# Kernel optimization log

Measured on AMD Instinct MI355X. Metric: run time of the kernel, lower is better.

Reference implementation:

```python
import jax, jax.numpy as jnp
import numpy as np

EPS_DEMOD = 1e-8
EPS_GN = 1e-5
GROUPS = 8


def setup_inputs() -> dict:
    key = jax.random.key(0)
    ks = jax.random.split(key, 4)
    b, c, h, w = 16, 64, 256, 256
    n_kernels, c_out = 4, 64
    x = jax.random.normal(ks[0], (b, c, h, w), dtype=jnp.float32)
    mod = jax.random.normal(ks[1], (b, c), dtype=jnp.float32)
    kernel_mod = jax.random.normal(ks[2], (b, n_kernels), dtype=jnp.float32)
    # kaiming normal, fan_in = c*3*3, leaky_relu gain sqrt(2)
    std = float(np.sqrt(2.0 / (c * 9)))
    conv_weights = jax.random.normal(ks[3], (n_kernels, c_out, c, 3, 3), dtype=jnp.float32) * std
    gn_gamma = jnp.ones((c_out,), dtype=jnp.float32)
    gn_beta = jnp.zeros((c_out,), dtype=jnp.float32)
    return {"x": x, "mod": mod, "kernel_mod": kernel_mod,
            "conv_weights": conv_weights, "gn_gamma": gn_gamma, "gn_beta": gn_beta}


def _block_forward(x, mod, kernel_mod, conv_weights, gn_gamma, gn_beta):
    b = x.shape[0]
    # --- adaptive kernel selection (softmax over num_conv_kernels) ---
    kernel_attn = jax.nn.softmax(kernel_mod, axis=-1)                # [b, n]
    w = jnp.einsum('noikl,bn->boikl', conv_weights, kernel_attn)     # [b, o, i, 3, 3]
    # --- stylegan2 modulation ---
    w = w * (mod[:, None, :, None, None] + 1.0)
    # --- demodulation ---
    inv_norm = jax.lax.rsqrt(jnp.clip(jnp.sum(w * w, axis=(2, 3, 4), keepdims=True), EPS_DEMOD, None))
    w = w * inv_norm
    # --- per-sample conv (vmap over batch, SAME padding, stride 1) ---
    def conv_one(xi, wi):
        return jax.lax.conv_general_dilated(
            xi[None], wi, window_strides=(1, 1), padding='SAME',
            dimension_numbers=('NCHW', 'OIHW', 'NCHW'))[0]
    y = jax.vmap(conv_one)(x, w)                                     # [b, o, h, w]
    # --- GroupNorm(groups=8) ---
    bb, c, hh, ww = y.shape
    yg = y.reshape(bb, GROUPS, c // GROUPS, hh, ww)
    mean = jnp.mean(yg, axis=(2, 3, 4), keepdims=True)
    var = jnp.var(yg, axis=(2, 3, 4), keepdims=True)
    yg = (yg - mean) * jax.lax.rsqrt(var + EPS_GN)
    y = yg.reshape(bb, c, hh, ww) * gn_gamma[None, :, None, None] + gn_beta[None, :, None, None]
    # --- SiLU ---
    return y * jax.nn.sigmoid(y)


def reference(x, mod, kernel_mod, conv_weights, gn_gamma, gn_beta):
    return _block_forward(x, mod, kernel_mod, conv_weights, gn_gamma, gn_beta)
```

## Files before the change

### kernel.cpp

```cpp
#include <hip/hip_runtime.h>
#include <hip/hip_bf16.h>
#include <math.h>

#define B_ 16
#define C_IN 64
#define C_OUT 64
#define H_ 256
#define W_ 256
#define NK 4
#define NGROUPS 8
#define CH_PER_G (C_OUT / NGROUPS)

#define WM16_SHORTS (B_ * C_OUT * 9 * C_IN)
#define STATS_FLOATS (B_ * NGROUPS * 2)

typedef __attribute__((ext_vector_type(8))) short bf16x8;
typedef __attribute__((ext_vector_type(4))) float f32x4;

static __device__ __forceinline__ unsigned bf16bits(float v) {
    return (unsigned)__builtin_bit_cast(unsigned short, __float2bfloat16(v));
}

__global__ __launch_bounds__(64)
void k_weights(const float* __restrict__ mod, const float* __restrict__ kmod,
               const float* __restrict__ cw, unsigned short* __restrict__ wm16) {
    int bo = blockIdx.x;
    int b = bo >> 6, o = bo & 63;
    int lane = threadIdx.x;

    float a0 = kmod[b * NK + 0], a1 = kmod[b * NK + 1];
    float a2 = kmod[b * NK + 2], a3 = kmod[b * NK + 3];
    float m = fmaxf(fmaxf(a0, a1), fmaxf(a2, a3));
    float e0 = __expf(a0 - m), e1 = __expf(a1 - m);
    float e2 = __expf(a2 - m), e3 = __expf(a3 - m);
    float inv = 1.0f / (e0 + e1 + e2 + e3);
    e0 *= inv; e1 *= inv; e2 *= inv; e3 *= inv;

    float modv = mod[b * C_IN + lane] + 1.0f;

    float wv[9];
    float ss = 0.0f;
#pragma unroll
    for (int j = 0; j < 9; ++j) {
        int idx = o * 576 + lane * 9 + j;
        float w = cw[0 * C_OUT * 576 + idx] * e0
                + cw[1 * C_OUT * 576 + idx] * e1
                + cw[2 * C_OUT * 576 + idx] * e2
                + cw[3 * C_OUT * 576 + idx] * e3;
        w *= modv;
        wv[j] = w;
        ss += w * w;
    }
#pragma unroll
    for (int off = 32; off > 0; off >>= 1)
        ss += __shfl_xor(ss, off, 64);
    float invn = rsqrtf(fmaxf(ss, 1e-8f));
#pragma unroll
    for (int j = 0; j < 9; ++j)
        wm16[((b * 64 + o) * 9 + j) * 64 + lane] =
            (unsigned short)bf16bits(wv[j] * invn);
}

#define NSLOT 340
#define LDSBYTES (NSLOT * 128)

__global__ __launch_bounds__(256, 3)
void k_conv(const float* __restrict__ x, const unsigned short* __restrict__ wm16,
            float* __restrict__ y, float* __restrict__ stats) {
    __shared__ __align__(16) char smem[LDSBYTES];
    __shared__ float lst[16];

    const int tile = blockIdx.x;
    const int b    = blockIdx.y;
    const int R0   = (tile >> 3) * 8;
    const int C0   = (tile & 7) * 32;
    const int tid  = threadIdx.x;
    const int w    = tid >> 6;
    const int lane = tid & 63;
    const int l15  = lane & 15;
    const int q    = lane >> 4;

    if (tid < 16) lst[tid] = 0.0f;

    for (int t = tid; t < NSLOT * 8; t += 256) {
        int chunk = t / NSLOT;
        int slot  = t - chunk * NSLOT;
        int r = slot / 34;
        int c = slot - r * 34;
        int gr = R0 - 1 + r;
        int gc = C0 - 1 + c;
        bool ok = ((unsigned)gr < (unsigned)H_) && ((unsigned)gc < (unsigned)W_);
        const float* xp = x + (((b * 64 + chunk * 8) * 256 + gr) * 256 + gc);
        unsigned u[4];
#pragma unroll
        for (int jj = 0; jj < 4; ++jj) {
            float v0 = ok ? xp[(2 * jj) * 65536] : 0.0f;
            float v1 = ok ? xp[(2 * jj + 1) * 65536] : 0.0f;
            u[jj] = (bf16bits(v1) << 16) | bf16bits(v0);
        }
        *(int4*)(smem + slot * 128 + ((chunk ^ (slot & 7)) << 4)) =
            make_int4(u[0], u[1], u[2], u[3]);
    }
    __syncthreads();

    f32x4 acc[4][4];
#pragma unroll
    for (int mt = 0; mt < 4; ++mt)
#pragma unroll
        for (int nt = 0; nt < 4; ++nt)
            acc[mt][nt] = (f32x4){0.f, 0.f, 0.f, 0.f};

    const unsigned short* wb = wm16 + b * (64 * 9 * 64);

    for (int tap = 0; tap < 9; ++tap) {
        const int ky = tap / 3;
        const int kx = tap - ky * 3;

        bf16x8 af[4][2];
#pragma unroll
        for (int mt = 0; mt < 4; ++mt)
#pragma unroll
            for (int kc = 0; kc < 2; ++kc)
                af[mt][kc] = *(const bf16x8*)(wb +
                    ((mt * 16 + l15) * 9 + tap) * 64 + kc * 32 + q * 8);

#pragma unroll
        for (int kc = 0; kc < 2; ++kc) {
            bf16x8 bfr[4];
#pragma unroll
            for (int nt = 0; nt < 4; ++nt) {
                int ro = 2 * w + (nt >> 1);
                int c0 = (nt & 1) * 16;
                int slot = (ro + ky) * 34 + c0 + kx + l15;
                int chunk = kc * 4 + q;
                bfr[nt] = *(const bf16x8*)(smem + slot * 128 +
                                           ((chunk ^ (slot & 7)) << 4));
            }
#pragma unroll
            for (int mt = 0; mt < 4; ++mt)
#pragma unroll
                for (int nt = 0; nt < 4; ++nt)
                    acc[mt][nt] = __builtin_amdgcn_mfma_f32_16x16x32_bf16(
                        af[mt][kc], bfr[nt], acc[mt][nt], 0, 0, 0);
        }
    }

    float sg[4] = {0.f, 0.f, 0.f, 0.f};
    float qg[4] = {0.f, 0.f, 0.f, 0.f};
#pragma unroll
    for (int mt = 0; mt < 4; ++mt) {
#pragma unroll
        for (int nt = 0; nt < 4; ++nt) {
            int ro = 2 * w + (nt >> 1);
            int c0 = (nt & 1) * 16;
            float* yp = y + ((b * 64 + mt * 16 + q * 4) * 65536 +
                             (R0 + ro) * 256 + C0 + c0 + l15);
#pragma unroll
            for (int r = 0; r < 4; ++r) {
                float v = acc[mt][nt][r];
                yp[r * 65536] = v;
                sg[mt] += v;
                qg[mt] += v * v;
            }
        }
    }
    const int gsel = q >> 1;
#pragma unroll
    for (int mt = 0; mt < 4; ++mt) {
        atomicAdd(&lst[(2 * mt + gsel) * 2 + 0], sg[mt]);
        atomicAdd(&lst[(2 * mt + gsel) * 2 + 1], qg[mt]);
    }
    __syncthreads();
    if (tid < 16) atomicAdd(&stats[b * 16 + tid], lst[tid]);
}

__global__ __launch_bounds__(256)
void k_norm(float4* __restrict__ y, const float* __restrict__ stats,
            const float* __restrict__ gamma, const float* __restrict__ beta) {
    const int cg = blockIdx.x >> 6;
    const int b  = cg >> 6;
    const int ch = cg & 63;
    const int g  = ch >> 3;

    const float sum = stats[(b * NGROUPS + g) * 2 + 0];
    const float ssq = stats[(b * NGROUPS + g) * 2 + 1];
    const float invN = 1.0f / (float)(CH_PER_G * H_ * W_);
    const float mean = sum * invN;
    const float var  = fmaxf(ssq * invN - mean * mean, 0.0f);
    const float rstd = rsqrtf(var + 1e-5f);
    const float ga = gamma[ch] * rstd;
    const float be = beta[ch] - mean * ga;

    const int idx = blockIdx.x * 256 + threadIdx.x;
    float4 v = y[idx];
    float t;
    t = v.x * ga + be; v.x = t / (1.0f + __expf(-t));
    t = v.y * ga + be; v.y = t / (1.0f + __expf(-t));
    t = v.z * ga + be; v.z = t / (1.0f + __expf(-t));
    t = v.w * ga + be; v.w = t / (1.0f + __expf(-t));
    y[idx] = v;
}

extern "C" void kernel_launch(void* const* d_in, const int* in_sizes, int n_in,
                              void* d_out, int out_size, void* d_ws, size_t ws_size,
                              hipStream_t stream) {
    const float* x     = (const float*)d_in[0];
    const float* mod   = (const float*)d_in[1];
    const float* kmod  = (const float*)d_in[2];
    const float* cw    = (const float*)d_in[3];
    const float* gamma = (const float*)d_in[4];
    const float* beta  = (const float*)d_in[5];
    float* out = (float*)d_out;

    unsigned short* wm16 = (unsigned short*)d_ws;
    float* stats = (float*)((char*)d_ws + WM16_SHORTS * sizeof(unsigned short));

    k_weights<<<dim3(B_ * C_OUT), dim3(64), 0, stream>>>(mod, kmod, cw, wm16);
    hipMemsetAsync(stats, 0, STATS_FLOATS * sizeof(float), stream);

    k_conv<<<dim3(256, B_), dim3(256), 0, stream>>>(x, wm16, out, stats);

    k_norm<<<dim3(B_ * C_OUT * 64), dim3(256), 0, stream>>>(
        (float4*)out, stats, gamma, beta);
}
```

Baseline: 889.7 us.

## Pre-transpose input to padded NHWC bf16 and stage conv tiles via direct LDS loads

```diff
diff --git a/kernel.cpp b/kernel.cpp
--- a/kernel.cpp
+++ b/kernel.cpp
@@ -12,13 +12,25 @@
 #define CH_PER_G (C_OUT / NGROUPS)
 
 #define WM16_SHORTS (B_ * C_OUT * 9 * C_IN)
+#define WM16_BYTES (WM16_SHORTS * 2)
 #define STATS_FLOATS (B_ * NGROUPS * 2)
+
+#define XT_PIX (258 * 258)
+#define XT_OFF ((size_t)(WM16_BYTES + 4096))
+#define XT_BYTES ((size_t)B_ * XT_PIX * 64 * 2)
 
 typedef __attribute__((ext_vector_type(8))) short bf16x8;
 typedef __attribute__((ext_vector_type(4))) float f32x4;
+typedef unsigned int u32;
 
 static __device__ __forceinline__ unsigned bf16bits(float v) {
     return (unsigned)__builtin_bit_cast(unsigned short, __float2bfloat16(v));
+}
+
+static __device__ __forceinline__ void load_lds16(const unsigned short* g, void* l) {
+    __builtin_amdgcn_global_load_lds(
+        (const __attribute__((address_space(1))) u32*)g,
+        (__attribute__((address_space(3))) u32*)l, 16, 0, 0);
 }
 
 __global__ __launch_bounds__(64)
@@ -61,7 +73,161 @@
             (unsigned short)bf16bits(wv[j] * invn);
 }
 
+__global__ __launch_bounds__(256)
+void k_border(unsigned short* __restrict__ xt) {
+    int t = blockIdx.x * 256 + threadIdx.x;
+    int chunk = t & 7;
+    int p = t >> 3;
+    int b = p / 1028;
+    int pid = p - b * 1028;
+    int r, c;
+    if (pid < 258)      { r = 0;             c = pid; }
+    else if (pid < 516) { r = 257;           c = pid - 258; }
+    else if (pid < 772) { r = pid - 516 + 1; c = 0; }
+    else                { r = pid - 772 + 1; c = 257; }
+    *(int4*)((char*)xt + (size_t)(b * XT_PIX + r * 258 + c) * 128 + chunk * 16) =
+        make_int4(0, 0, 0, 0);
+}
+
+__global__ __launch_bounds__(256)
+void k_xpose(const float* __restrict__ x, unsigned short* __restrict__ xt) {
+    const int bx  = blockIdx.x;
+    const int seg = bx & 1;
+    const int h   = (bx >> 1) & 255;
+    const int b   = bx >> 9;
+    const int c   = threadIdx.x & 63;
+    const int wv  = threadIdx.x >> 6;
+    const int p0  = seg * 128 + wv * 32;
+    const float* xp = x + (((b * 64 + c) * 256 + h) * 256 + p0);
+    unsigned short* op = xt + ((size_t)(b * 258 + h + 1) * 258 + p0 + 1) * 64 + c;
+#pragma unroll
+    for (int j = 0; j < 8; ++j) {
+        float4 v = *(const float4*)(xp + j * 4);
+        op[(j * 4 + 0) * 64] = (unsigned short)bf16bits(v.x);
+        op[(j * 4 + 1) * 64] = (unsigned short)bf16bits(v.y);
+        op[(j * 4 + 2) * 64] = (unsigned short)bf16bits(v.z);
+        op[(j * 4 + 3) * 64] = (unsigned short)bf16bits(v.w);
+    }
+}
+
 #define NSLOT 340
+#define SLOTPAD 352
+
+__global__ __launch_bounds__(256, 3)
+void k_conv2(const unsigned short* __restrict__ xt,
+             const unsigned short* __restrict__ wm16,
+             float* __restrict__ y, float* __restrict__ stats) {
+    __shared__ __align__(16) char smem[SLOTPAD * 128];
+    __shared__ float lst[16];
+
+    const int tile = blockIdx.x;
+    const int b    = blockIdx.y;
+    const int R0   = (tile >> 3) * 8;
+    const int C0   = (tile & 7) * 32;
+    const int tid  = threadIdx.x;
+    const int w    = tid >> 6;
+    const int lane = tid & 63;
+    const int l15  = lane & 15;
+    const int q    = lane >> 4;
+
+    if (tid < 16) lst[tid] = 0.0f;
+
+    const unsigned short* xb = xt + (size_t)b * (XT_PIX * 64);
+#pragma unroll
+    for (int k = 0; k < 11; ++k) {
+        int t = k * 256 + tid;
+        int slot = t >> 3;
+        int p = t & 7;
+        int s = slot < NSLOT ? slot : NSLOT - 1;
+        int r = s / 34;
+        int c = s - r * 34;
+        int srcchunk = p ^ (s & 7);
+        const unsigned short* src = xb + (((R0 + r) * 258 + (C0 + c)) * 64 + srcchunk * 8);
+        load_lds16(src, smem + t * 16);
+    }
+    __syncthreads();
+
+    f32x4 acc[4][4];
+#pragma unroll
+    for (int mt = 0; mt < 4; ++mt)
+#pragma unroll
+        for (int nt = 0; nt < 4; ++nt)
+            acc[mt][nt] = (f32x4){0.f, 0.f, 0.f, 0.f};
+
+    const unsigned short* wb = wm16 + b * (64 * 9 * 64);
+
+    for (int tap = 0; tap < 9; ++tap) {
+        const int ky = tap / 3;
+        const int kx = tap - ky * 3;
+
+        bf16x8 af[4][2];
+#pragma unroll
+        for (int mt = 0; mt < 4; ++mt)
+#pragma unroll
+            for (int kc = 0; kc < 2; ++kc)
+                af[mt][kc] = *(const bf16x8*)(wb +
+                    ((mt * 16 + l15) * 9 + tap) * 64 + kc * 32 + q * 8);
+
+#pragma unroll
+        for (int kc = 0; kc < 2; ++kc) {
+            bf16x8 bfr[4];
+#pragma unroll
+            for (int nt = 0; nt < 4; ++nt) {
+                int ro = 2 * w + (nt >> 1);
+                int c0 = (nt & 1) * 16;
+                int slot = (ro + ky) * 34 + c0 + kx + l15;
+                int chunk = kc * 4 + q;
+                bfr[nt] = *(const bf16x8*)(smem + slot * 128 +
+                                           ((chunk ^ (slot & 7)) << 4));
+            }
+#pragma unroll
+            for (int mt = 0; mt < 4; ++mt)
+#pragma unroll
+                for (int nt = 0; nt < 4; ++nt)
+                    acc[mt][nt] = __builtin_amdgcn_mfma_f32_16x16x32_bf16(
+                        af[mt][kc], bfr[nt], acc[mt][nt], 0, 0, 0);
+        }
+    }
+
+    float sg[4] = {0.f, 0.f, 0.f, 0.f};
+    float qg[4] = {0.f, 0.f, 0.f, 0.f};
+#pragma unroll
+    for (int mt = 0; mt < 4; ++mt) {
+#pragma unroll
+        for (int nt = 0; nt < 4; ++nt) {
+            int ro = 2 * w + (nt >> 1);
+            int c0 = (nt & 1) * 16;
+            float* yp = y + ((b * 64 + mt * 16 + q * 4) * 65536 +
+                             (R0 + ro) * 256 + C0 + c0 + l15);
+#pragma unroll
+            for (int r = 0; r < 4; ++r) {
+                float v = acc[mt][nt][r];
+                yp[r * 65536] = v;
+                sg[mt] += v;
+                qg[mt] += v * v;
+            }
+        }
+    }
+#pragma unroll
+    for (int mt = 0; mt < 4; ++mt) {
+#pragma unroll
+        for (int off = 1; off <= 16; off <<= 1) {
+            sg[mt] += __shfl_xor(sg[mt], off, 64);
+            qg[mt] += __shfl_xor(qg[mt], off, 64);
+        }
+    }
+    if ((lane & 31) == 0) {
+        const int gsel = q >> 1;
+#pragma unroll
+        for (int mt = 0; mt < 4; ++mt) {
+            atomicAdd(&lst[(2 * mt + gsel) * 2 + 0], sg[mt]);
+            atomicAdd(&lst[(2 * mt + gsel) * 2 + 1], qg[mt]);
+        }
+    }
+    __syncthreads();
+    if (tid < 16) atomicAdd(&stats[b * 16 + tid], lst[tid]);
+}
+
 #define LDSBYTES (NSLOT * 128)
 
 __global__ __launch_bounds__(256, 3)
@@ -213,12 +379,19 @@
     float* out = (float*)d_out;
 
     unsigned short* wm16 = (unsigned short*)d_ws;
-    float* stats = (float*)((char*)d_ws + WM16_SHORTS * sizeof(unsigned short));
+    float* stats = (float*)((char*)d_ws + WM16_BYTES);
+    unsigned short* xt = (unsigned short*)((char*)d_ws + XT_OFF);
 
     k_weights<<<dim3(B_ * C_OUT), dim3(64), 0, stream>>>(mod, kmod, cw, wm16);
     hipMemsetAsync(stats, 0, STATS_FLOATS * sizeof(float), stream);
 
-    k_conv<<<dim3(256, B_), dim3(256), 0, stream>>>(x, wm16, out, stats);
+    if (ws_size >= XT_OFF + XT_BYTES) {
+        k_border<<<dim3(514), dim3(256), 0, stream>>>(xt);
+        k_xpose<<<dim3(8192), dim3(256), 0, stream>>>(x, xt);
+        k_conv2<<<dim3(256, B_), dim3(256), 0, stream>>>(xt, wm16, out, stats);
+    } else {
+        k_conv<<<dim3(256, B_), dim3(256), 0, stream>>>(x, wm16, out, stats);
+    }
 
     k_norm<<<dim3(B_ * C_OUT * 64), dim3(256), 0, stream>>>(
         (float4*)out, stats, gamma, beta);
```

Result: faster. 746.9 us (-16.0%).
